# Kernel tuning notes

Hardware: AMD Instinct MI355X
Metric: run time of the kernel (lower is better)

## Reference

```python
import jax, jax.numpy as jnp
import numpy as np

B, LQ, LK, D = 64, 1024, 1024, 64
TEMPERATURE = 8.0  # sqrt(D)


def setup_inputs() -> dict:
    key = jax.random.key(0)
    k1, k2, k3, k4, k5, k6 = jax.random.split(key, 6)
    query = jax.random.normal(k1, (B, LQ, D), dtype=jnp.float32)
    key_t = jax.random.normal(k2, (B, LK, D), dtype=jnp.float32)
    value = jax.random.normal(k3, (B, LK, D), dtype=jnp.float32)
    query_mask = jax.random.uniform(k4, (B, LQ)) > 0.1
    key_mask = jax.random.uniform(k5, (B, LK)) > 0.1
    mask = jax.random.uniform(k6, (B, LQ, LK)) > 0.1
    return {"query": query, "key": key_t, "value": value,
            "query_mask": query_mask, "key_mask": key_mask, "mask": mask}


def reference(query, key, value, query_mask, key_mask, mask):
    # unnormalized score: bmm + scale + key/general masking with -inf
    attn = jnp.einsum('bqd,bkd->bqk', query, key) / TEMPERATURE
    neg_inf = jnp.array(-jnp.inf, dtype=attn.dtype)
    if key_mask is not None:
        attn = jnp.where(key_mask[:, None, :], attn, neg_inf)
    if mask is not None:
        attn = jnp.where(mask, attn, neg_inf)
    # softmax over key dim, then zero out masked queries
    attn = jax.nn.softmax(attn, axis=2)
    if query_mask is not None:
        attn = jnp.where(query_mask[:, :, None], attn, 0.0)
    attn_value = jnp.einsum('bqk,bkd->bqd', attn, value)
    return attn_value, attn
```

## Files before the change

### kernel.cpp

```cpp
#include <hip/hip_runtime.h>
#include <hip/hip_bf16.h>


#define NB   64
#define SLQ  1024
#define SLK  1024
#define DH   64
#define TQ   16
#define TK   64
#define NKT  16
#define KSTR 80
#define VSTR 76
#define PSTR 40

typedef __attribute__((ext_vector_type(4))) float          f32x4;
typedef __attribute__((ext_vector_type(8))) __bf16         bf16x8;
typedef __attribute__((ext_vector_type(8))) unsigned short u16x8;
typedef __attribute__((ext_vector_type(4))) unsigned short u16x4;

static __device__ __forceinline__ unsigned short f2bf(float f) {
  union { float f; unsigned u; } c; c.f = f;
  unsigned u = c.u;
  u += 0x7fffu + ((u >> 16) & 1u);
  return (unsigned short)(u >> 16);
}
static __device__ __forceinline__ u16x4 cvt4(f32x4 v) {
  u16x4 h; h[0]=f2bf(v[0]); h[1]=f2bf(v[1]); h[2]=f2bf(v[2]); h[3]=f2bf(v[3]);
  return h;
}

__global__ __launch_bounds__(256, 3) void sdpa_fused(
    const float* __restrict__ Q, const float* __restrict__ K,
    const float* __restrict__ V, const int* __restrict__ QM,
    const int* __restrict__ KM, const int* __restrict__ MSK,
    float* __restrict__ OUT_AV, float* __restrict__ OUT_P) {
  const int g    = blockIdx.x;
  const int slot = g >> 3;
  const int b    = ((slot >> 6) << 3) | (g & 7);
  const int q0   = (slot & 63) * TQ;

  const int tid  = threadIdx.x;
  const int wave = tid >> 6;
  const int lane = tid & 63;
  const int col  = lane & 15;
  const int quad = lane >> 4;
  const int lrow = lane >> 4;
  const int lc4  = (lane & 15) * 4;

  __shared__ __align__(16) unsigned char RAW[25216];
  unsigned short* Kw = (unsigned short*)RAW + wave * (16 * KSTR);
  unsigned short* Vw = (unsigned short*)RAW + wave * (32 * VSTR);
  float*          Ow = (float*)(RAW + wave * (32 * VSTR * 2));
  unsigned short* Pw = (unsigned short*)(RAW + 19456) + wave * (16 * PSTR);
  float* partM = (float*)(RAW + 24576);
  float* partL = partM + 64;
  float* rowM  = partL + 64;
  float* rowS  = rowM + 16;

  const f32x4* kb4 = (const f32x4*)(K + (size_t)b * SLK * DH);
  const f32x4* vb4 = (const f32x4*)(V + (size_t)b * SLK * DH);
  const size_t mbase = ((size_t)b * SLQ + q0) * SLK;

  const float* qp = Q + ((size_t)b * SLQ + q0 + col) * DH + quad * 8;
  bf16x8 aq0, aq1;
  {
    u16x4 a = cvt4(*(const f32x4*)qp),        c = cvt4(*(const f32x4*)(qp + 4));
    u16x4 d = cvt4(*(const f32x4*)(qp + 32)), e = cvt4(*(const f32x4*)(qp + 36));
    u16x8 h0, h1;
#pragma unroll
    for (int j = 0; j < 4; ++j) { h0[j]=a[j]; h0[j+4]=c[j]; h1[j]=d[j]; h1[j+4]=e[j]; }
    aq0 = __builtin_bit_cast(bf16x8, h0);
    aq1 = __builtin_bit_cast(bf16x8, h1);
  }

  float sreg[NKT][4];
  float mloc[4] = {-INFINITY, -INFINITY, -INFINITY, -INFINITY};
  float lloc[4] = {0.f, 0.f, 0.f, 0.f};

  f32x4 kreg[4];
#pragma unroll
  for (int j = 0; j < 4; ++j)
    kreg[j] = kb4[(size_t)(wave * 16 + j * 4 + lrow) * 16 + (lane & 15)];
  int km_c = KM[b * SLK + wave * 16 + col];
  int msk_c[4];
#pragma unroll
  for (int r = 0; r < 4; ++r)
    msk_c[r] = MSK[mbase + (size_t)(quad * 4 + r) * SLK + wave * 16 + col];

#pragma unroll
  for (int kt = 0; kt < NKT; ++kt) {
#pragma unroll
    for (int j = 0; j < 4; ++j)
      *(u16x4*)&Kw[(j * 4 + lrow) * KSTR + lc4] = cvt4(kreg[j]);

    int km_n = 0, msk_n[4] = {0, 0, 0, 0};
    if (kt < NKT - 1) {
      const int brow = (kt + 1) * TK + wave * 16;
#pragma unroll
      for (int j = 0; j < 4; ++j)
        kreg[j] = kb4[(size_t)(brow + j * 4 + lrow) * 16 + (lane & 15)];
      km_n = KM[b * SLK + brow + col];
#pragma unroll
      for (int r = 0; r < 4; ++r)
        msk_n[r] = MSK[mbase + (size_t)(quad * 4 + r) * SLK + brow + col];
    }

    bf16x8 bk0 = __builtin_bit_cast(bf16x8, *(const u16x8*)&Kw[col * KSTR + quad * 8]);
    bf16x8 bk1 = __builtin_bit_cast(bf16x8, *(const u16x8*)&Kw[col * KSTR + quad * 8 + 32]);
    f32x4 acc = {0.f, 0.f, 0.f, 0.f};
    acc = __builtin_amdgcn_mfma_f32_16x16x32_bf16(aq0, bk0, acc, 0, 0, 0);
    acc = __builtin_amdgcn_mfma_f32_16x16x32_bf16(aq1, bk1, acc, 0, 0, 0);

#pragma unroll
    for (int r = 0; r < 4; ++r) {
      float s = (km_c && msk_c[r]) ? acc[r] * 0.125f : -INFINITY;
      sreg[kt][r] = s;
      float mn = fmaxf(mloc[r], s);
      if (mn != -INFINITY) {
        lloc[r] = lloc[r] * __expf(mloc[r] - mn) + __expf(s - mn);
        mloc[r] = mn;
      }
    }
    km_c = km_n;
#pragma unroll
    for (int r = 0; r < 4; ++r) msk_c[r] = msk_n[r];
  }

  f32x4 vreg[8];
#pragma unroll
  for (int j = 0; j < 8; ++j)
    vreg[j] = vb4[(size_t)((j >> 2) * TK + wave * 16 + (j & 3) * 4 + lrow) * 16 + (lane & 15)];

#pragma unroll
  for (int r = 0; r < 4; ++r) {
#pragma unroll
    for (int off = 1; off < 16; off <<= 1) {
      float om = __shfl_xor(mloc[r], off, 64);
      float ol = __shfl_xor(lloc[r], off, 64);
      float mn = fmaxf(mloc[r], om);
      if (mn != -INFINITY) {
        lloc[r] = lloc[r] * __expf(mloc[r] - mn) + ol * __expf(om - mn);
        mloc[r] = mn;
      }
    }
  }
  if (col == 0) {
#pragma unroll
    for (int r = 0; r < 4; ++r) {
      partM[wave * 16 + quad * 4 + r] = mloc[r];
      partL[wave * 16 + quad * 4 + r] = lloc[r];
    }
  }
  __syncthreads();
  if (tid < TQ) {
    float M = -INFINITY, L = 0.f;
#pragma unroll
    for (int w = 0; w < 4; ++w) {
      float m_ = partM[w * 16 + tid], l_ = partL[w * 16 + tid];
      float mn = fmaxf(M, m_);
      if (mn != -INFINITY) {
        L = L * __expf(M - mn) + l_ * __expf(m_ - mn);
        M = mn;
      }
    }
    rowM[tid] = M;
    rowS[tid] = QM[b * SLQ + q0 + tid] ? (1.f / L) : 0.f;
  }
  __syncthreads();

  float Mr[4], Sr[4];
#pragma unroll
  for (int r = 0; r < 4; ++r) { Mr[r] = rowM[quad * 4 + r]; Sr[r] = rowS[quad * 4 + r]; }

  f32x4 acco[4] = {{0.f,0.f,0.f,0.f},{0.f,0.f,0.f,0.f},{0.f,0.f,0.f,0.f},{0.f,0.f,0.f,0.f}};
#pragma unroll
  for (int st = 0; st < 8; ++st) {
    const int kt0 = st * 2, kt1 = st * 2 + 1;
#pragma unroll
    for (int j = 0; j < 8; ++j)
      *(u16x4*)&Vw[(j * 4 + lrow) * VSTR + lc4] = cvt4(vreg[j]);

    float p0[4], p1[4];
#pragma unroll
    for (int r = 0; r < 4; ++r) {
      p0[r] = __expf(sreg[kt0][r] - Mr[r]) * Sr[r];
      p1[r] = __expf(sreg[kt1][r] - Mr[r]) * Sr[r];
      Pw[(quad * 4 + r) * PSTR + col]      = f2bf(p0[r]);
      Pw[(quad * 4 + r) * PSTR + 16 + col] = f2bf(p1[r]);
    }
#pragma unroll
    for (int r = 0; r < 4; ++r) {
      OUT_P[mbase + (size_t)(quad * 4 + r) * SLK + kt0 * TK + wave * 16 + col] = p0[r];
      OUT_P[mbase + (size_t)(quad * 4 + r) * SLK + kt1 * TK + wave * 16 + col] = p1[r];
    }

    if (st < 7) {
#pragma unroll
      for (int j = 0; j < 8; ++j)
        vreg[j] = vb4[(size_t)((st * 2 + 2 + (j >> 2)) * TK + wave * 16 + (j & 3) * 4 + lrow) * 16
                      + (lane & 15)];
    }

    bf16x8 ap = __builtin_bit_cast(bf16x8, *(const u16x8*)&Pw[col * PSTR + quad * 8]);
#pragma unroll
    for (int n0 = 0; n0 < 4; ++n0) {
      u16x8 rv;
#pragma unroll
      for (int j = 0; j < 8; ++j)
        rv[j] = Vw[(quad * 8 + j) * VSTR + n0 * 16 + col];
      acco[n0] = __builtin_amdgcn_mfma_f32_16x16x32_bf16(
          ap, __builtin_bit_cast(bf16x8, rv), acco[n0], 0, 0, 0);
    }
  }

#pragma unroll
  for (int n0 = 0; n0 < 4; ++n0)
#pragma unroll
    for (int r = 0; r < 4; ++r)
      Ow[(quad * 4 + r) * 64 + n0 * 16 + col] = acco[n0][r];
  __syncthreads();
  {
    const int qq = tid >> 4, dd = (tid & 15) * 4;
    f32x4 s = {0.f, 0.f, 0.f, 0.f};
#pragma unroll
    for (int w = 0; w < 4; ++w) {
      const float* Os = (const float*)(RAW + w * (32 * VSTR * 2));
      f32x4 t = *(const f32x4*)&Os[qq * 64 + dd];
      s += t;
    }
    *(f32x4*)&OUT_AV[((size_t)b * SLQ + q0 + qq) * DH + dd] = s;
  }
}

extern "C" void kernel_launch(void* const* d_in, const int* in_sizes, int n_in,
                              void* d_out, int out_size, void* d_ws, size_t ws_size,
                              hipStream_t stream) {
  const float* q  = (const float*)d_in[0];
  const float* k  = (const float*)d_in[1];
  const float* v  = (const float*)d_in[2];
  const int*   qm = (const int*)d_in[3];
  const int*   km = (const int*)d_in[4];
  const int*   mk = (const int*)d_in[5];
  float* out_av = (float*)d_out;
  float* out_p  = out_av + (size_t)NB * SLQ * DH;
  sdpa_fused<<<dim3(NB * (SLQ / TQ)), dim3(256), 0, stream>>>(q, k, v, qm, km, mk, out_av, out_p);
}
```

Baseline: 592.4 us.

## Load K/V directly into MFMA registers, two-pass softmax, nontemporal mask and output traffic

Drops the LDS staging of K and V. Each lane now loads its MFMA operand fragments straight from global memory and converts them to bf16 with the native cast. The online max/sum softmax is replaced by a two-pass version: a register max, then exp and sum. The exponentials are kept in registers so the second phase only rescales them, and the 1/8 temperature is folded into Q. Mask reads and the P and AV output writes use nontemporal hints. This removes LDS round-trips and the per-tile exp recomputation, but V is now gathered with strided scalar loads and the software prefetch of K and V is gone.

Result: slower. 667.8 us (+12.7%).

```diff
diff --git a/kernel.cpp b/kernel.cpp
--- a/kernel.cpp
+++ b/kernel.cpp
@@ -9,24 +9,21 @@
 #define TQ   16
 #define TK   64
 #define NKT  16
-#define KSTR 80
-#define VSTR 76
 #define PSTR 40
+#define OSTR 68
 
 typedef __attribute__((ext_vector_type(4))) float          f32x4;
 typedef __attribute__((ext_vector_type(8))) __bf16         bf16x8;
 typedef __attribute__((ext_vector_type(8))) unsigned short u16x8;
-typedef __attribute__((ext_vector_type(4))) unsigned short u16x4;
 
 static __device__ __forceinline__ unsigned short f2bf(float f) {
-  union { float f; unsigned u; } c; c.f = f;
-  unsigned u = c.u;
-  u += 0x7fffu + ((u >> 16) & 1u);
-  return (unsigned short)(u >> 16);
-}
-static __device__ __forceinline__ u16x4 cvt4(f32x4 v) {
-  u16x4 h; h[0]=f2bf(v[0]); h[1]=f2bf(v[1]); h[2]=f2bf(v[2]); h[3]=f2bf(v[3]);
-  return h;
+  return __builtin_bit_cast(unsigned short, (__bf16)f);
+}
+static __device__ __forceinline__ bf16x8 cvt8(f32x4 a, f32x4 b) {
+  bf16x8 r;
+#pragma unroll
+  for (int i = 0; i < 4; ++i) { r[i] = (__bf16)a[i]; r[i + 4] = (__bf16)b[i]; }
+  return r;
 }
 
 __global__ __launch_bounds__(256, 3) void sdpa_fused(
@@ -44,111 +41,77 @@
   const int lane = tid & 63;
   const int col  = lane & 15;
   const int quad = lane >> 4;
-  const int lrow = lane >> 4;
-  const int lc4  = (lane & 15) * 4;
-
-  __shared__ __align__(16) unsigned char RAW[25216];
-  unsigned short* Kw = (unsigned short*)RAW + wave * (16 * KSTR);
-  unsigned short* Vw = (unsigned short*)RAW + wave * (32 * VSTR);
-  float*          Ow = (float*)(RAW + wave * (32 * VSTR * 2));
-  unsigned short* Pw = (unsigned short*)(RAW + 19456) + wave * (16 * PSTR);
-  float* partM = (float*)(RAW + 24576);
+
+  __shared__ __align__(16) unsigned char RAW[23168];
+  float*          Ow = (float*)RAW + wave * (16 * OSTR);
+  unsigned short* Pw = (unsigned short*)(RAW + 17408) + wave * (16 * PSTR);
+  float* partM = (float*)(RAW + 22528);
   float* partL = partM + 64;
   float* rowM  = partL + 64;
   float* rowS  = rowM + 16;
 
-  const f32x4* kb4 = (const f32x4*)(K + (size_t)b * SLK * DH);
-  const f32x4* vb4 = (const f32x4*)(V + (size_t)b * SLK * DH);
   const size_t mbase = ((size_t)b * SLQ + q0) * SLK;
 
   const float* qp = Q + ((size_t)b * SLQ + q0 + col) * DH + quad * 8;
   bf16x8 aq0, aq1;
   {
-    u16x4 a = cvt4(*(const f32x4*)qp),        c = cvt4(*(const f32x4*)(qp + 4));
-    u16x4 d = cvt4(*(const f32x4*)(qp + 32)), e = cvt4(*(const f32x4*)(qp + 36));
-    u16x8 h0, h1;
-#pragma unroll
-    for (int j = 0; j < 4; ++j) { h0[j]=a[j]; h0[j+4]=c[j]; h1[j]=d[j]; h1[j+4]=e[j]; }
-    aq0 = __builtin_bit_cast(bf16x8, h0);
-    aq1 = __builtin_bit_cast(bf16x8, h1);
-  }
+    f32x4 a = *(const f32x4*)qp        * 0.125f;
+    f32x4 c = *(const f32x4*)(qp + 4)  * 0.125f;
+    f32x4 d = *(const f32x4*)(qp + 32) * 0.125f;
+    f32x4 e = *(const f32x4*)(qp + 36) * 0.125f;
+    aq0 = cvt8(a, c);
+    aq1 = cvt8(d, e);
+  }
+
+  const float* kp  = K + ((size_t)b * SLK + wave * 16 + col) * DH + quad * 8;
+  const int*   kmp = KM + b * SLK + wave * 16 + col;
+  const int*   mkp = MSK + mbase + (size_t)(quad * 4) * SLK + wave * 16 + col;
 
   float sreg[NKT][4];
-  float mloc[4] = {-INFINITY, -INFINITY, -INFINITY, -INFINITY};
-  float lloc[4] = {0.f, 0.f, 0.f, 0.f};
-
-  f32x4 kreg[4];
-#pragma unroll
-  for (int j = 0; j < 4; ++j)
-    kreg[j] = kb4[(size_t)(wave * 16 + j * 4 + lrow) * 16 + (lane & 15)];
-  int km_c = KM[b * SLK + wave * 16 + col];
-  int msk_c[4];
-#pragma unroll
-  for (int r = 0; r < 4; ++r)
-    msk_c[r] = MSK[mbase + (size_t)(quad * 4 + r) * SLK + wave * 16 + col];
-
 #pragma unroll
   for (int kt = 0; kt < NKT; ++kt) {
-#pragma unroll
-    for (int j = 0; j < 4; ++j)
-      *(u16x4*)&Kw[(j * 4 + lrow) * KSTR + lc4] = cvt4(kreg[j]);
-
-    int km_n = 0, msk_n[4] = {0, 0, 0, 0};
-    if (kt < NKT - 1) {
-      const int brow = (kt + 1) * TK + wave * 16;
-#pragma unroll
-      for (int j = 0; j < 4; ++j)
-        kreg[j] = kb4[(size_t)(brow + j * 4 + lrow) * 16 + (lane & 15)];
-      km_n = KM[b * SLK + brow + col];
-#pragma unroll
-      for (int r = 0; r < 4; ++r)
-        msk_n[r] = MSK[mbase + (size_t)(quad * 4 + r) * SLK + brow + col];
-    }
-
-    bf16x8 bk0 = __builtin_bit_cast(bf16x8, *(const u16x8*)&Kw[col * KSTR + quad * 8]);
-    bf16x8 bk1 = __builtin_bit_cast(bf16x8, *(const u16x8*)&Kw[col * KSTR + quad * 8 + 32]);
+    const float* kq = kp + (size_t)kt * (TK * DH);
+    f32x4 k0 = *(const f32x4*)kq;
+    f32x4 k1 = *(const f32x4*)(kq + 4);
+    f32x4 k2 = *(const f32x4*)(kq + 32);
+    f32x4 k3 = *(const f32x4*)(kq + 36);
+    const int km = kmp[kt * TK];
+    int mr[4];
+#pragma unroll
+    for (int r = 0; r < 4; ++r)
+      mr[r] = __builtin_nontemporal_load(mkp + (size_t)r * SLK + kt * TK);
+    bf16x8 bk0 = cvt8(k0, k1);
+    bf16x8 bk1 = cvt8(k2, k3);
     f32x4 acc = {0.f, 0.f, 0.f, 0.f};
     acc = __builtin_amdgcn_mfma_f32_16x16x32_bf16(aq0, bk0, acc, 0, 0, 0);
     acc = __builtin_amdgcn_mfma_f32_16x16x32_bf16(aq1, bk1, acc, 0, 0, 0);
-
-#pragma unroll
-    for (int r = 0; r < 4; ++r) {
-      float s = (km_c && msk_c[r]) ? acc[r] * 0.125f : -INFINITY;
-      sreg[kt][r] = s;
-      float mn = fmaxf(mloc[r], s);
-      if (mn != -INFINITY) {
-        lloc[r] = lloc[r] * __expf(mloc[r] - mn) + __expf(s - mn);
-        mloc[r] = mn;
-      }
-    }
-    km_c = km_n;
-#pragma unroll
-    for (int r = 0; r < 4; ++r) msk_c[r] = msk_n[r];
-  }
-
-  f32x4 vreg[8];
-#pragma unroll
-  for (int j = 0; j < 8; ++j)
-    vreg[j] = vb4[(size_t)((j >> 2) * TK + wave * 16 + (j & 3) * 4 + lrow) * 16 + (lane & 15)];
-
+#pragma unroll
+    for (int r = 0; r < 4; ++r)
+      sreg[kt][r] = (km && mr[r]) ? acc[r] : -INFINITY;
+  }
+
+  float Mw[4], Cr[4];
 #pragma unroll
   for (int r = 0; r < 4; ++r) {
-#pragma unroll
-    for (int off = 1; off < 16; off <<= 1) {
-      float om = __shfl_xor(mloc[r], off, 64);
-      float ol = __shfl_xor(lloc[r], off, 64);
-      float mn = fmaxf(mloc[r], om);
-      if (mn != -INFINITY) {
-        lloc[r] = lloc[r] * __expf(mloc[r] - mn) + ol * __expf(om - mn);
-        mloc[r] = mn;
-      }
-    }
-  }
-  if (col == 0) {
-#pragma unroll
-    for (int r = 0; r < 4; ++r) {
-      partM[wave * 16 + quad * 4 + r] = mloc[r];
-      partL[wave * 16 + quad * 4 + r] = lloc[r];
+    float m = sreg[0][r];
+#pragma unroll
+    for (int kt = 1; kt < NKT; ++kt) m = fmaxf(m, sreg[kt][r]);
+#pragma unroll
+    for (int off = 1; off < 16; off <<= 1) m = fmaxf(m, __shfl_xor(m, off, 64));
+    Mw[r] = m;
+    const float mc = fmaxf(m, -1e30f);
+    float l = 0.f;
+#pragma unroll
+    for (int kt = 0; kt < NKT; ++kt) {
+      float e = __expf(sreg[kt][r] - mc);
+      sreg[kt][r] = e;
+      l += e;
+    }
+#pragma unroll
+    for (int off = 1; off < 16; off <<= 1) l += __shfl_xor(l, off, 64);
+    if (col == 0) {
+      partM[wave * 16 + quad * 4 + r] = Mw[r];
+      partL[wave * 16 + quad * 4 + r] = l;
     }
   }
   __syncthreads();
@@ -163,53 +126,52 @@
         M = mn;
       }
     }
-    rowM[tid] = M;
-    rowS[tid] = QM[b * SLQ + q0 + tid] ? (1.f / L) : 0.f;
+    rowM[tid] = fmaxf(M, -1e30f);
+    rowS[tid] = (QM[b * SLQ + q0 + tid] && L > 0.f) ? (1.f / L) : 0.f;
   }
   __syncthreads();
-
-  float Mr[4], Sr[4];
-#pragma unroll
-  for (int r = 0; r < 4; ++r) { Mr[r] = rowM[quad * 4 + r]; Sr[r] = rowS[quad * 4 + r]; }
-
-  f32x4 acco[4] = {{0.f,0.f,0.f,0.f},{0.f,0.f,0.f,0.f},{0.f,0.f,0.f,0.f},{0.f,0.f,0.f,0.f}};
+#pragma unroll
+  for (int r = 0; r < 4; ++r)
+    Cr[r] = __expf(fmaxf(Mw[r], -1e30f) - rowM[quad * 4 + r]) * rowS[quad * 4 + r];
+
+  const float* vp = V + ((size_t)b * SLK + wave * 16 + (quad & 1) * 8 +
+                         (quad >> 1) * TK) * DH + col;
+  float* outp = OUT_P + mbase + (size_t)(quad * 4) * SLK + wave * 16 + col;
+
+  f32x4 acco[4] = {{0.f,0.f,0.f,0.f},{0.f,0.f,0.f,0.f},
+                   {0.f,0.f,0.f,0.f},{0.f,0.f,0.f,0.f}};
 #pragma unroll
   for (int st = 0; st < 8; ++st) {
-    const int kt0 = st * 2, kt1 = st * 2 + 1;
-#pragma unroll
-    for (int j = 0; j < 8; ++j)
-      *(u16x4*)&Vw[(j * 4 + lrow) * VSTR + lc4] = cvt4(vreg[j]);
-
+    const int kt0 = st * 2, kt1 = kt0 + 1;
     float p0[4], p1[4];
 #pragma unroll
     for (int r = 0; r < 4; ++r) {
-      p0[r] = __expf(sreg[kt0][r] - Mr[r]) * Sr[r];
-      p1[r] = __expf(sreg[kt1][r] - Mr[r]) * Sr[r];
+      p0[r] = sreg[kt0][r] * Cr[r];
+      p1[r] = sreg[kt1][r] * Cr[r];
       Pw[(quad * 4 + r) * PSTR + col]      = f2bf(p0[r]);
       Pw[(quad * 4 + r) * PSTR + 16 + col] = f2bf(p1[r]);
     }
 #pragma unroll
     for (int r = 0; r < 4; ++r) {
-      OUT_P[mbase + (size_t)(quad * 4 + r) * SLK + kt0 * TK + wave * 16 + col] = p0[r];
-      OUT_P[mbase + (size_t)(quad * 4 + r) * SLK + kt1 * TK + wave * 16 + col] = p1[r];
-    }
-
-    if (st < 7) {
+      __builtin_nontemporal_store(p0[r], outp + (size_t)r * SLK + kt0 * TK);
+      __builtin_nontemporal_store(p1[r], outp + (size_t)r * SLK + kt1 * TK);
+    }
+
+    const float* vq = vp + (size_t)st * (2 * TK * DH);
+    float vv[4][8];
+#pragma unroll
+    for (int n0 = 0; n0 < 4; ++n0)
 #pragma unroll
       for (int j = 0; j < 8; ++j)
-        vreg[j] = vb4[(size_t)((st * 2 + 2 + (j >> 2)) * TK + wave * 16 + (j & 3) * 4 + lrow) * 16
-                      + (lane & 15)];
-    }
+        vv[n0][j] = vq[(size_t)j * DH + n0 * 16];
 
     bf16x8 ap = __builtin_bit_cast(bf16x8, *(const u16x8*)&Pw[col * PSTR + quad * 8]);
 #pragma unroll
     for (int n0 = 0; n0 < 4; ++n0) {
-      u16x8 rv;
-#pragma unroll
-      for (int j = 0; j < 8; ++j)
-        rv[j] = Vw[(quad * 8 + j) * VSTR + n0 * 16 + col];
-      acco[n0] = __builtin_amdgcn_mfma_f32_16x16x32_bf16(
-          ap, __builtin_bit_cast(bf16x8, rv), acco[n0], 0, 0, 0);
+      bf16x8 bv;
+#pragma unroll
+      for (int j = 0; j < 8; ++j) bv[j] = (__bf16)vv[n0][j];
+      acco[n0] = __builtin_amdgcn_mfma_f32_16x16x32_bf16(ap, bv, acco[n0], 0, 0, 0);
     }
   }
 
@@ -217,18 +179,17 @@
   for (int n0 = 0; n0 < 4; ++n0)
 #pragma unroll
     for (int r = 0; r < 4; ++r)
-      Ow[(quad * 4 + r) * 64 + n0 * 16 + col] = acco[n0][r];
+      Ow[(quad * 4 + r) * OSTR + n0 * 16 + col] = acco[n0][r];
   __syncthreads();
   {
     const int qq = tid >> 4, dd = (tid & 15) * 4;
     f32x4 s = {0.f, 0.f, 0.f, 0.f};
 #pragma unroll
     for (int w = 0; w < 4; ++w) {
-      const float* Os = (const float*)(RAW + w * (32 * VSTR * 2));
-      f32x4 t = *(const f32x4*)&Os[qq * 64 + dd];
-      s += t;
-    }
-    *(f32x4*)&OUT_AV[((size_t)b * SLQ + q0 + qq) * DH + dd] = s;
+      const float* Os = (const float*)RAW + w * (16 * OSTR);
+      s += *(const f32x4*)&Os[qq * OSTR + dd];
+    }
+    __builtin_nontemporal_store(s, (f32x4*)&OUT_AV[((size_t)b * SLQ + q0 + qq) * DH + dd]);
   }
 }
 
```
